# Kernel tuning notes

Measured on AMD Instinct MI355X. Metric: run time of the kernel, lower is better.

The kernel has to match this reference:

```python
import jax, jax.numpy as jnp
import numpy as np

B, T, E, H, D = 256, 77, 1280, 20, 64
SCALE = D ** -0.5
NEG = -1e9


def setup_inputs() -> dict:
    key = jax.random.key(0)
    ks = jax.random.split(key, 32)
    w = lambda k, shape, s=0.02: jax.random.normal(k, shape, dtype=jnp.float32) * s
    causal = jnp.triu(jnp.full((T, T), NEG, dtype=jnp.float32), k=1)
    causal_mask = jnp.broadcast_to(causal[None, None], (B, 1, T, T))
    return {
        'hidden_states': jax.random.normal(ks[0], (B, T, E), dtype=jnp.float32),
        'embeds': jax.random.normal(ks[1], (B, T, E), dtype=jnp.float32),
        'causal_mask': causal_mask,
        'q_w': w(ks[2], (E, E)), 'q_b': w(ks[3], (E,)),
        'k_w': w(ks[4], (E, E)), 'k_b': w(ks[5], (E,)),
        'v_w': w(ks[6], (E, E)), 'v_b': w(ks[7], (E,)),
        'o_w': w(ks[8], (E, E)), 'o_b': w(ks[9], (E,)),
        'ka_w': w(ks[10], (E, E)) * 0.01, 'ka_b': w(ks[11], (E,)) * 0.001,
        'va_w': w(ks[12], (E, E)) * 0.01, 'va_b': w(ks[13], (E,)) * 0.001,
        'zc1_w': w(ks[14], (E, E)), 'zc1_b': w(ks[15], (E,)),
        'zt1_w': w(ks[16], (T, 2 * T)), 'zt1_b': w(ks[17], (T,)),
        'zc2_w': w(ks[18], (E, E)), 'zc2_b': w(ks[19], (E,)),
        'zt2_w': w(ks[20], (T, T)), 'zt2_b': w(ks[21], (T,)),
    }


def _heads(x):
    # (B, S, E) -> (B, H, S, D)
    return x.reshape(B, -1, H, D).transpose(0, 2, 1, 3)


def _attend(q, k, v, mask=None):
    # q,k,v: (B,H,*,D); returns (B,T,E)
    logits = jnp.einsum('bhtd,bhsd->bhts', q, k)
    if mask is not None:
        logits = logits + mask  # mask: (B,1,T,S)
    probs = jax.nn.softmax(logits, axis=-1)  # dropout p=0 in eval
    ctx = jnp.einsum('bhts,bhsd->bhtd', probs, v)
    return ctx.transpose(0, 2, 1, 3).reshape(B, T, E)


def _zipper(x, zc1_w, zc1_b, zt1_w, zt1_b, zc2_w, zc2_b, zt2_w, zt2_b):
    # token/channel mixer: (B, 2T, E) -> (B, T, E)
    x = jax.nn.gelu(x @ zc1_w.T + zc1_b)              # channel: E -> hidden E
    x = jnp.swapaxes(x, 1, 2)                          # (B, E, 2T)
    x = jax.nn.gelu(x @ zt1_w.T + zt1_b)               # tokens: 2T -> T
    x = jnp.swapaxes(x, 1, 2)                          # (B, T, E)
    x = x @ zc2_w.T + zc2_b                            # channel: E -> E
    x = jnp.swapaxes(x, 1, 2) @ zt2_w.T + zt2_b        # tokens: T -> T
    return jnp.swapaxes(x, 1, 2)


def reference(hidden_states, embeds, causal_mask,
              q_w, q_b, k_w, k_b, v_w, v_b, o_w, o_b,
              ka_w, ka_b, va_w, va_b,
              zc1_w, zc1_b, zt1_w, zt1_b, zc2_w, zc2_b, zt2_w, zt2_b):
    q = _heads((hidden_states @ q_w.T + q_b) * SCALE)
    k = _heads(hidden_states @ k_w.T + k_b)
    v = _heads(hidden_states @ v_w.T + v_b)
    attn_output = _attend(q, k, v, causal_mask)  # self-attention pass

    # adapter cross-attention pass (shared query)
    ka = _heads(embeds @ ka_w.T + ka_b)
    va = _heads(embeds @ va_w.T + va_b)
    attn_output_adapter = _attend(q, ka, va, None)

    zipped = _zipper(jnp.concatenate([attn_output_adapter, attn_output], axis=1),
                     zc1_w, zc1_b, zt1_w, zt1_b, zc2_w, zc2_b, zt2_w, zt2_b)
    attn_output = attn_output + zipped
    return attn_output @ o_w.T + o_b
```

## Files before the change

kernel.cpp:

```cpp
#include <hip/hip_runtime.h>
#include <stdint.h>

#define B_    256
#define T_    77
#define E_    1280
#define H_    20
#define T2_   154
#define MTOK  19712
#define MTOK2 39424

typedef float f32x4 __attribute__((ext_vector_type(4)));
typedef short bf16x8 __attribute__((ext_vector_type(8)));

__device__ inline float bf2f(short s) {
    return __uint_as_float(((unsigned)(unsigned short)s) << 16);
}
__device__ inline short f2bf(float f) {
    unsigned u = __float_as_uint(f);
    u += 0x7fff + ((u >> 16) & 1);
    return (short)(u >> 16);
}
__device__ inline float gelu_tanh(float x) {
    float x3 = x * x * x;
    return 0.5f * x * (1.0f + tanhf(0.7978845608028654f * (x + 0.044715f * x3)));
}

__global__ void cast_f32_bf16(const float* __restrict__ in, short* __restrict__ out, int n4) {
    int i = blockIdx.x * blockDim.x + threadIdx.x;
    int stride = gridDim.x * blockDim.x;
    for (; i < n4; i += stride) {
        float4 v = reinterpret_cast<const float4*>(in)[i];
        short4 o;
        o.x = f2bf(v.x); o.y = f2bf(v.y); o.z = f2bf(v.z); o.w = f2bf(v.w);
        reinterpret_cast<short4*>(out)[i] = o;
    }
}

__global__ void cast8_f32_bf16(const float* __restrict__ s0, const float* __restrict__ s1,
                               const float* __restrict__ s2, const float* __restrict__ s3,
                               const float* __restrict__ s4, const float* __restrict__ s5,
                               const float* __restrict__ s6, const float* __restrict__ s7,
                               short* __restrict__ out) {
    const int per = E_ * E_ / 4;
    int i = blockIdx.x * blockDim.x + threadIdx.x;
    int stride = gridDim.x * blockDim.x;
    for (; i < 8 * per; i += stride) {
        int w = i / per, j = i - w * per;
        const float* src = w == 0 ? s0 : w == 1 ? s1 : w == 2 ? s2 : w == 3 ? s3
                         : w == 4 ? s4 : w == 5 ? s5 : w == 6 ? s6 : s7;
        float4 v = reinterpret_cast<const float4*>(src)[j];
        short4 o;
        o.x = f2bf(v.x); o.y = f2bf(v.y); o.z = f2bf(v.z); o.w = f2bf(v.w);
        reinterpret_cast<short4*>(out)[i] = o;
    }
}

__global__ void pad_weight(const float* __restrict__ W, short* __restrict__ Wp,
                           int rows, int cols, int KP) {
    int i = blockIdx.x * 256 + threadIdx.x;
    if (i >= 80 * KP) return;
    int t = i / KP, s = i - t * KP;
    Wp[i] = (t < rows && s < cols) ? f2bf(W[t * cols + s]) : (short)0;
}

template<int NSEG, int EPI>
__global__ __launch_bounds__(512, 2)
void qgemm(const short* __restrict__ A, const short* __restrict__ W,
           const float* __restrict__ b0, const float* __restrict__ b1,
           const float* __restrict__ b2,
           short* __restrict__ o0, short* __restrict__ o1, short* __restrict__ o2,
           float s0) {
    const int K = E_;
    const int NT = K / 64;
    __shared__ short As[2 * 2 * 8192];
    __shared__ short Bs[2 * 2 * 8192];
    const int tid = threadIdx.x;
    const int wave = tid >> 6, lane = tid & 63;
    const int wr = wave >> 2, wc = wave & 3;

    const int nwg = gridDim.x;
    const int qq = nwg >> 3, rr = nwg & 7;
    const int x = blockIdx.x & 7, ii = blockIdx.x >> 3;
    const int L = (x < rr ? x * (qq + 1) : rr * (qq + 1) + (x - rr) * qq) + ii;
    const int PB = nwg / NSEG;
    const int seg = L / PB;
    const int rem = L - seg * PB;
    const int bm = rem / 5, bnl = rem % 5;

    const long arow0 = (long)bm * 256;
    const long brow0 = (long)seg * E_ + bnl * 256;

    const int rsub = lane >> 3;
    const int colswz = (((lane & 7) ^ rsub) & 7) * 8;
    const int swz = (lane & 7) << 3;

    f32x4 acc[8][4] = {};

    auto STAGE_A = [&](int par, int half, int kt) {
#pragma unroll
        for (int i = 0; i < 2; ++i) {
            int chunk = i * 8 + wave;
            int row = chunk * 8 + rsub;
            const short* ga = A + (arow0 + half * 128 + row) * K + kt * 64 + colswz;
            __builtin_amdgcn_global_load_lds(
                (const __attribute__((address_space(1))) unsigned int*)ga,
                (__attribute__((address_space(3))) unsigned int*)
                    &As[par * 16384 + half * 8192 + chunk * 512], 16, 0, 0);
        }
    };
    auto STAGE_B = [&](int par, int half, int kt) {
#pragma unroll
        for (int i = 0; i < 2; ++i) {
            int chunk = i * 8 + wave;
            int row = chunk * 8 + rsub;
            const short* gb = W + (brow0 + half * 128 + row) * K + kt * 64 + colswz;
            __builtin_amdgcn_global_load_lds(
                (const __attribute__((address_space(1))) unsigned int*)gb,
                (__attribute__((address_space(3))) unsigned int*)
                    &Bs[par * 16384 + half * 8192 + chunk * 512], 16, 0, 0);
        }
    };

    bf16x8 Afr[4][2], Bfr[2][2];
    auto LDA = [&](int par, int hm) {
#pragma unroll
        for (int mi = 0; mi < 4; ++mi)
#pragma unroll
            for (int kk = 0; kk < 2; ++kk)
                Afr[mi][kk] = *reinterpret_cast<const bf16x8*>(
                    &As[par * 16384 + hm * 8192 +
                        (((wr * 64 + mi * 16 + (lane & 15)) * 64 + kk * 32 +
                          (lane >> 4) * 8) ^ swz)]);
    };
    auto LDB = [&](int par, int hn) {
#pragma unroll
        for (int nj = 0; nj < 2; ++nj)
#pragma unroll
            for (int kk = 0; kk < 2; ++kk)
                Bfr[nj][kk] = *reinterpret_cast<const bf16x8*>(
                    &Bs[par * 16384 + hn * 8192 +
                        (((wc * 32 + nj * 16 + (lane & 15)) * 64 + kk * 32 +
                          (lane >> 4) * 8) ^ swz)]);
    };
    auto MFMA16 = [&](int hm, int hn) {
        __builtin_amdgcn_s_setprio(1);
#pragma unroll
        for (int mi = 0; mi < 4; ++mi)
#pragma unroll
            for (int nj = 0; nj < 2; ++nj)
#pragma unroll
                for (int kk = 0; kk < 2; ++kk)
                    acc[hm * 4 + mi][hn * 2 + nj] =
                        __builtin_amdgcn_mfma_f32_16x16x32_bf16(
                            Afr[mi][kk], Bfr[nj][kk], acc[hm * 4 + mi][hn * 2 + nj],
                            0, 0, 0);
        __builtin_amdgcn_s_setprio(0);
    };

    STAGE_A(0, 0, 0); STAGE_B(0, 0, 0); STAGE_B(0, 1, 0); STAGE_A(0, 1, 0);

    for (int t = 0; t < NT - 1; ++t) {
        const int par = t & 1, nxt = par ^ 1;
        asm volatile("s_waitcnt vmcnt(4)" ::: "memory");
        __builtin_amdgcn_s_barrier(); __builtin_amdgcn_sched_barrier(0);
        LDA(par, 0); LDB(par, 0);
        STAGE_A(nxt, 0, t + 1);
        MFMA16(0, 0);
        asm volatile("s_waitcnt vmcnt(4)" ::: "memory");
        __builtin_amdgcn_s_barrier(); __builtin_amdgcn_sched_barrier(0);
        LDB(par, 1);
        STAGE_B(nxt, 0, t + 1);
        MFMA16(0, 1);
        asm volatile("s_waitcnt vmcnt(4)" ::: "memory");
        __builtin_amdgcn_s_barrier(); __builtin_amdgcn_sched_barrier(0);
        LDA(par, 1); LDB(par, 0);
        STAGE_B(nxt, 1, t + 1);
        MFMA16(1, 0);
        __builtin_amdgcn_s_barrier(); __builtin_amdgcn_sched_barrier(0);
        LDB(par, 1);
        STAGE_A(nxt, 1, t + 1);
        MFMA16(1, 1);
    }
    {
        const int par = (NT - 1) & 1;
        asm volatile("s_waitcnt vmcnt(4)" ::: "memory");
        __builtin_amdgcn_s_barrier(); __builtin_amdgcn_sched_barrier(0);
        LDA(par, 0); LDB(par, 0);
        MFMA16(0, 0);
        asm volatile("s_waitcnt vmcnt(2)" ::: "memory");
        __builtin_amdgcn_s_barrier(); __builtin_amdgcn_sched_barrier(0);
        LDB(par, 1);
        MFMA16(0, 1);
        asm volatile("s_waitcnt vmcnt(0)" ::: "memory");
        __builtin_amdgcn_s_barrier(); __builtin_amdgcn_sched_barrier(0);
        LDA(par, 1); LDB(par, 0);
        MFMA16(1, 0);
        __builtin_amdgcn_s_barrier(); __builtin_amdgcn_sched_barrier(0);
        LDB(par, 1);
        MFMA16(1, 1);
    }

    const float* bias = seg == 0 ? b0 : (seg == 1 ? b1 : b2);
    short* out = seg == 0 ? o0 : (seg == 1 ? o1 : o2);
    const float scl = (EPI == 0 && seg == 0) ? s0 : 1.f;
#pragma unroll
    for (int hm = 0; hm < 2; ++hm)
#pragma unroll
        for (int mi = 0; mi < 4; ++mi)
#pragma unroll
            for (int hn = 0; hn < 2; ++hn)
#pragma unroll
                for (int nj = 0; nj < 2; ++nj) {
                    int ncol = bnl * 256 + hn * 128 + wc * 32 + nj * 16 + (lane & 15);
                    float bv = bias[ncol];
#pragma unroll
                    for (int r = 0; r < 4; ++r) {
                        long grow = arow0 + hm * 128 + wr * 64 + mi * 16 +
                                    (lane >> 4) * 4 + r;
                        float v = acc[hm * 4 + mi][hn * 2 + nj][r] + bv;
                        if (EPI == 2) v = gelu_tanh(v);
                        else v *= scl;
                        out[grow * E_ + ncol] = f2bf(v);
                    }
                }
}

#define GEMM_CORE(A_, W_, KDIM, ACC)                                                   \
    const int rsub = lane >> 3;                                                        \
    const int col  = (((lane & 7) ^ rsub) & 7) * 8;                                    \
    const int swz  = (lane & 7) << 3;                                                  \
    for (int kt = 0; kt < (KDIM); kt += 64) {                                          \
        __syncthreads();                                                               \
        _Pragma("unroll")                                                              \
        for (int i = 0; i < 4; ++i) {                                                  \
            int chunk = i * 4 + wave;                                                  \
            int row = chunk * 8 + rsub;                                                \
            const short* ga = (A_) + (arow0 + row) * (KDIM) + kt + col;                \
            const short* gb = (W_) + (brow0 + row) * (KDIM) + kt + col;                \
            __builtin_amdgcn_global_load_lds(                                          \
                (const __attribute__((address_space(1))) unsigned int*)ga,             \
                (__attribute__((address_space(3))) unsigned int*)&Als[chunk * 512],    \
                16, 0, 0);                                                             \
            __builtin_amdgcn_global_load_lds(                                          \
                (const __attribute__((address_space(1))) unsigned int*)gb,             \
                (__attribute__((address_space(3))) unsigned int*)&Bls[chunk * 512],    \
                16, 0, 0);                                                             \
        }                                                                              \
        __syncthreads();                                                               \
        _Pragma("unroll")                                                              \
        for (int kk = 0; kk < 2; ++kk) {                                               \
            bf16x8 af[4], bfr[4];                                                      \
            _Pragma("unroll")                                                          \
            for (int mi = 0; mi < 4; ++mi)                                             \
                af[mi] = *reinterpret_cast<const bf16x8*>(                             \
                    &Als[(((wm + mi * 16 + (lane & 15)) * 64 + kk * 32 +               \
                           (lane >> 4) * 8)) ^ swz]);                                  \
            _Pragma("unroll")                                                          \
            for (int nj = 0; nj < 4; ++nj)                                             \
                bfr[nj] = *reinterpret_cast<const bf16x8*>(                            \
                    &Bls[(((wn + nj * 16 + (lane & 15)) * 64 + kk * 32 +               \
                           (lane >> 4) * 8)) ^ swz]);                                  \
            _Pragma("unroll")                                                          \
            for (int mi = 0; mi < 4; ++mi)                                             \
                _Pragma("unroll")                                                      \
                for (int nj = 0; nj < 4; ++nj)                                         \
                    ACC[mi][nj] = __builtin_amdgcn_mfma_f32_16x16x32_bf16(             \
                        af[mi], bfr[nj], ACC[mi][nj], 0, 0, 0);                        \
        }                                                                              \
    }

template<int EPI>
__global__ void gemm_bt(const short* __restrict__ A, const short* __restrict__ W,
                        const float* __restrict__ bias, void* __restrict__ Cout,
                        int K) {
    const int N = E_;
    const int NBN = E_ / 128;
    __shared__ short Als[128 * 64];
    __shared__ short Bls[128 * 64];
    const int tid  = threadIdx.x;
    const int wave = tid >> 6, lane = tid & 63;

    const int nwg = gridDim.x;
    const int qq = nwg >> 3, rr = nwg & 7;
    const int x = blockIdx.x & 7, ii = blockIdx.x >> 3;
    const int L = (x < rr ? x * (qq + 1) : rr * (qq + 1) + (x - rr) * qq) + ii;
    const int bm = L / NBN, bn = L % NBN;

    const int wm = (wave >> 1) * 64, wn = (wave & 1) * 64;
    f32x4 acc[4][4] = {};
    const long arow0 = (long)bm * 128;
    const long brow0 = (long)bn * 128;

    GEMM_CORE(A, W, K, acc)

#pragma unroll
    for (int mi = 0; mi < 4; ++mi) {
#pragma unroll
        for (int nj = 0; nj < 4; ++nj) {
            int gcol = bn * 128 + wn + nj * 16 + (lane & 15);
            float bv = bias[gcol];
#pragma unroll
            for (int r = 0; r < 4; ++r) {
                long grow = arow0 + wm + mi * 16 + (lane >> 4) * 4 + r;
                float v = acc[mi][nj][r] + bv;
                if (EPI == 3) ((float*)Cout)[grow * N + gcol] = v;
                else          ((short*)Cout)[grow * N + gcol] = f2bf(v);
            }
        }
    }
}

template<int SIN, int KP, int PS, bool GELU, bool RESID>
__global__ void mixer_mfma(const short* __restrict__ IN, const short* __restrict__ Wp,
                           const float* __restrict__ bias, const short* __restrict__ Cat,
                           short* __restrict__ OUT) {
    __shared__ short lsT[64 * PS];
    const int e0 = blockIdx.x * 64;
    const int b  = blockIdx.y;
    const int tid = threadIdx.x, wave = tid >> 6, lane = tid & 63;

    const int eg = tid & 7;
    const int sl = tid >> 3;
    for (int sb = sl; sb < KP; sb += 32) {
        if (sb < SIN) {
            bf16x8 v = *reinterpret_cast<const bf16x8*>(
                &IN[((long)b * SIN + sb) * E_ + e0 + eg * 8]);
#pragma unroll
            for (int i = 0; i < 8; ++i)
                lsT[(eg * 8 + i) * PS + sb] = v[i];
        } else {
#pragma unroll
            for (int i = 0; i < 8; ++i)
                lsT[(eg * 8 + i) * PS + sb] = 0;
        }
    }
    __syncthreads();

    const int ebase = wave * 16;
    f32x4 acc[5] = {};
#pragma unroll
    for (int ks = 0; ks < KP / 32; ++ks) {
        bf16x8 bfr = *reinterpret_cast<const bf16x8*>(
            &lsT[(ebase + (lane & 15)) * PS + ks * 32 + (lane >> 4) * 8]);
#pragma unroll
        for (int mt = 0; mt < 5; ++mt) {
            bf16x8 af = *reinterpret_cast<const bf16x8*>(
                &Wp[(mt * 16 + (lane & 15)) * KP + ks * 32 + (lane >> 4) * 8]);
            acc[mt] = __builtin_amdgcn_mfma_f32_16x16x32_bf16(af, bfr, acc[mt], 0, 0, 0);
        }
    }

    const int e = e0 + ebase + (lane & 15);
#pragma unroll
    for (int mt = 0; mt < 5; ++mt) {
#pragma unroll
        for (int r = 0; r < 4; ++r) {
            int t = mt * 16 + (lane >> 4) * 4 + r;
            if (t < T_) {
                float v = acc[mt][r] + bias[t];
                if (GELU) v = gelu_tanh(v);
                if (RESID) v += bf2f(Cat[((long)b * T2_ + T_ + t) * E_ + e]);
                OUT[((long)b * T_ + t) * E_ + e] = f2bf(v);
            }
        }
    }
}

#define ASTR 104
__global__ __launch_bounds__(64, 1)
void attn_mfma(const short* __restrict__ Qm,
               const short* __restrict__ Km, const short* __restrict__ Vm,
               const short* __restrict__ KAm, const short* __restrict__ VAm,
               short* __restrict__ Cat) {
    __shared__ short pls[80 * ASTR];
    __shared__ short vt[64 * ASTR];
    const int hh = blockIdx.x;
    const int b = hh / H_, h = hh % H_;
    const int lane = threadIdx.x & 63;
    const int colbase = lane & 15, g = lane >> 4;
    const long base = ((long)b * T_) * E_ + h * 64;

    for (int pass = 0; pass < 2; ++pass) {
        const short* Kp = pass ? KAm : Km;
        const short* Vp = pass ? VAm : Vm;
        const bool causal = (pass == 0);
        const int rowoff = pass ? 0 : T_;

        {
            int4 z = {0, 0, 0, 0};
#pragma unroll
            for (int it = 0; it < 4; ++it) {
                int idx = it * 64 + lane;
                int row = idx >> 2, cb = idx & 3;
                *reinterpret_cast<int4*>(&vt[row * ASTR + 64 + cb * 8]) = z;
            }
#pragma unroll
            for (int it = 0; it < 3; ++it) {
                int idx = it * 64 + lane;
                if (idx < 160) {
                    int row = idx >> 1, cb = idx & 1;
                    *reinterpret_cast<int4*>(&pls[row * ASTR + 80 + cb * 8]) = z;
                }
            }
        }

        {
            const short* vb = Vp + base + (long)lane * E_;
#pragma unroll
            for (int dg = 0; dg < 8; ++dg) {
                bf16x8 v = *reinterpret_cast<const bf16x8*>(vb + dg * 8);
#pragma unroll
                for (int i = 0; i < 8; ++i) vt[(dg * 8 + i) * ASTR + lane] = v[i];
            }
            if (lane < T_ - 64) {
                const short* vb2 = Vp + base + (long)(64 + lane) * E_;
#pragma unroll
                for (int dg = 0; dg < 8; ++dg) {
                    bf16x8 v = *reinterpret_cast<const bf16x8*>(vb2 + dg * 8);
#pragma unroll
                    for (int i = 0; i < 8; ++i) vt[(dg * 8 + i) * ASTR + 64 + lane] = v[i];
                }
            }
        }

        f32x4 sacc[5][5] = {};
#pragma unroll
        for (int kk = 0; kk < 2; ++kk) {
            bf16x8 qf[5];
#pragma unroll
            for (int mi = 0; mi < 5; ++mi) {
                int t = mi * 16 + colbase; t = t > 76 ? 76 : t;
                qf[mi] = *reinterpret_cast<const bf16x8*>(
                    Qm + base + (long)t * E_ + kk * 32 + g * 8);
            }
#pragma unroll
            for (int nj = 0; nj < 5; ++nj) {
                int s = nj * 16 + colbase; s = s > 76 ? 76 : s;
                bf16x8 kf = *reinterpret_cast<const bf16x8*>(
                    Kp + base + (long)s * E_ + kk * 32 + g * 8);
#pragma unroll
                for (int mi = 0; mi < 5; ++mi)
                    sacc[mi][nj] = __builtin_amdgcn_mfma_f32_16x16x32_bf16(
                        qf[mi], kf, sacc[mi][nj], 0, 0, 0);
            }
        }

        float inv[5][4];
#pragma unroll
        for (int mi = 0; mi < 5; ++mi) {
#pragma unroll
            for (int r = 0; r < 4; ++r) {
                int t = mi * 16 + g * 4 + r;
                float mx = -3.0e38f;
#pragma unroll
                for (int nj = 0; nj < 5; ++nj) {
                    int s = nj * 16 + colbase;
                    bool ok = causal ? (s <= t) : (s < T_);
                    if (ok) mx = fmaxf(mx, sacc[mi][nj][r]);
                }
#pragma unroll
                for (int o = 1; o <= 8; o <<= 1) mx = fmaxf(mx, __shfl_xor(mx, o));
                float sum = 0.f;
#pragma unroll
                for (int nj = 0; nj < 5; ++nj) {
                    int s = nj * 16 + colbase;
                    bool ok = causal ? (s <= t) : (s < T_);
                    float pv = ok ? __expf(sacc[mi][nj][r] - mx) : 0.f;
                    sacc[mi][nj][r] = pv;
                    sum += pv;
                }
#pragma unroll
                for (int o = 1; o <= 8; o <<= 1) sum += __shfl_xor(sum, o);
                inv[mi][r] = 1.0f / sum;
            }
        }

#pragma unroll
        for (int mi = 0; mi < 5; ++mi)
#pragma unroll
            for (int nj = 0; nj < 5; ++nj)
#pragma unroll
                for (int r = 0; r < 4; ++r)
                    pls[(mi * 16 + g * 4 + r) * ASTR + nj * 16 + colbase] =
                        f2bf(sacc[mi][nj][r]);

        f32x4 cacc[5][4] = {};
#pragma unroll
        for (int ks = 0; ks < 3; ++ks) {
            bf16x8 pa[5];
#pragma unroll
            for (int mi = 0; mi < 5; ++mi)
                pa[mi] = *reinterpret_cast<const bf16x8*>(
                    &pls[(mi * 16 + colbase) * ASTR + ks * 32 + g * 8]);
#pragma unroll
            for (int nd = 0; nd < 4; ++nd) {
                bf16x8 vf = *reinterpret_cast<const bf16x8*>(
                    &vt[(nd * 16 + colbase) * ASTR + ks * 32 + g * 8]);
#pragma unroll
                for (int mi = 0; mi < 5; ++mi)
                    cacc[mi][nd] = __builtin_amdgcn_mfma_f32_16x16x32_bf16(
                        pa[mi], vf, cacc[mi][nd], 0, 0, 0);
            }
        }

#pragma unroll
        for (int mi = 0; mi < 5; ++mi)
#pragma unroll
            for (int nd = 0; nd < 4; ++nd)
#pragma unroll
                for (int r = 0; r < 4; ++r) {
                    int t = mi * 16 + g * 4 + r;
                    if (t < T_) {
                        float val = cacc[mi][nd][r] * inv[mi][r];
                        Cat[((long)b * T2_ + rowoff + t) * E_ + h * 64 + nd * 16 + colbase] =
                            f2bf(val);
                    }
                }
    }
}

extern "C" void kernel_launch(void* const* d_in, const int* in_sizes, int n_in,
                              void* d_out, int out_size, void* d_ws, size_t ws_size,
                              hipStream_t stream) {
    const float* hidden = (const float*)d_in[0];
    const float* embeds = (const float*)d_in[1];
    const float* q_w  = (const float*)d_in[3];  const float* q_b  = (const float*)d_in[4];
    const float* k_w  = (const float*)d_in[5];  const float* k_b  = (const float*)d_in[6];
    const float* v_w  = (const float*)d_in[7];  const float* v_b  = (const float*)d_in[8];
    const float* o_w  = (const float*)d_in[9];  const float* o_b  = (const float*)d_in[10];
    const float* ka_w = (const float*)d_in[11]; const float* ka_b = (const float*)d_in[12];
    const float* va_w = (const float*)d_in[13]; const float* va_b = (const float*)d_in[14];
    const float* zc1_w = (const float*)d_in[15]; const float* zc1_b = (const float*)d_in[16];
    const float* zt1_w = (const float*)d_in[17]; const float* zt1_b = (const float*)d_in[18];
    const float* zc2_w = (const float*)d_in[19]; const float* zc2_b = (const float*)d_in[20];
    const float* zt2_w = (const float*)d_in[21]; const float* zt2_b = (const float*)d_in[22];

    char* ws = (char*)d_ws;
    const size_t WSZ = (size_t)E_ * E_ * 2;
    const size_t ASZ = (size_t)MTOK * E_ * 2;
    short* Wq  = (short*)(ws + 0 * WSZ);
    short* Wka = (short*)(ws + 3 * WSZ);
    short* Wz1 = (short*)(ws + 5 * WSZ);
    short* Wz2 = (short*)(ws + 6 * WSZ);
    short* Wo  = (short*)(ws + 7 * WSZ);
    char* p = ws + 8 * WSZ;
    short* Ahs  = (short*)p; p += ASZ;
    short* Aemb = (short*)p; p += ASZ;
    short* Qb   = (short*)p; p += ASZ;
    short* Kb   = (short*)p; p += ASZ;
    short* Vb   = (short*)p; p += ASZ;
    short* KAb  = (short*)p; p += ASZ;
    short* VAb  = (short*)p; p += ASZ;
    short* Wz1p = (short*)p; p += 80 * 160 * 2;
    short* Wz2p = (short*)p; p += 80 * 96 * 2;
    short* CAT = Ahs;
    short* Y   = KAb;
    short* X2  = Qb;
    short* X3  = Kb;
    short* S   = Vb;

    if (ws_size < (size_t)(p - ws)) return;

    cast_f32_bf16<<<2048, 256, 0, stream>>>(hidden, Ahs,  MTOK * E_ / 4);
    cast_f32_bf16<<<2048, 256, 0, stream>>>(embeds, Aemb, MTOK * E_ / 4);
    cast8_f32_bf16<<<2048, 256, 0, stream>>>(q_w, k_w, v_w, ka_w, va_w, zc1_w, zc2_w, o_w,
                                             Wq);
    pad_weight<<<(80 * 160 + 255) / 256, 256, 0, stream>>>(zt1_w, Wz1p, 77, 154, 160);
    pad_weight<<<(80 * 96 + 255) / 256, 256, 0, stream>>>(zt2_w, Wz2p, 77, 77, 96);

    const int gQKV  = (MTOK / 256) * (3 * E_ / 256);
    const int gKAVA = (MTOK / 256) * (2 * E_ / 256);
    const int gZC1  = (MTOK2 / 256) * (E_ / 256);
    const int g154  = (MTOK / 128) * (E_ / 128);
    qgemm<3, 0><<<gQKV, 512, 0, stream>>>(Ahs, Wq, q_b, k_b, v_b,
                                          Qb, Kb, Vb, 0.125f);
    qgemm<2, 0><<<gKAVA, 512, 0, stream>>>(Aemb, Wka, ka_b, va_b, va_b,
                                           KAb, VAb, VAb, 1.f);
    attn_mfma<<<B_ * H_, 64, 0, stream>>>(Qb, Kb, Vb, KAb, VAb, CAT);
    qgemm<1, 2><<<gZC1, 512, 0, stream>>>(CAT, Wz1, zc1_b, zc1_b, zc1_b,
                                          Y, Y, Y, 1.f);
    mixer_mfma<154, 160, 168, true, false><<<dim3(E_ / 64, B_), 256, 0, stream>>>(
        Y, Wz1p, zt1_b, nullptr, X2);
    gemm_bt<0><<<g154, 256, 0, stream>>>(X2, Wz2, zc2_b, X3, E_);
    mixer_mfma<77, 96, 104, false, true><<<dim3(E_ / 64, B_), 256, 0, stream>>>(
        X3, Wz2p, zt2_b, CAT, S);
    gemm_bt<3><<<g154, 256, 0, stream>>>(S, Wo, o_b, (float*)d_out, E_);
}
```

Baseline: 1.154 ms.

## Double-buffer A/B register fragments and reorder quadrant MFMAs to cut LDS reloads

```diff
diff --git a/kernel.cpp b/kernel.cpp
--- a/kernel.cpp
+++ b/kernel.cpp
@@ -95,6 +95,7 @@
     const int swz = (lane & 7) << 3;
 
     f32x4 acc[8][4] = {};
+    bf16x8 AfA[4][2], AfB[4][2], Bf0[2][2], Bf1[2][2];
 
     auto STAGE_A = [&](int par, int half, int kt) {
 #pragma unroll
@@ -120,29 +121,27 @@
                     &Bs[par * 16384 + half * 8192 + chunk * 512], 16, 0, 0);
         }
     };
-
-    bf16x8 Afr[4][2], Bfr[2][2];
-    auto LDA = [&](int par, int hm) {
+    auto LDA = [&](bf16x8 (&dst)[4][2], int par, int hm) {
 #pragma unroll
         for (int mi = 0; mi < 4; ++mi)
 #pragma unroll
             for (int kk = 0; kk < 2; ++kk)
-                Afr[mi][kk] = *reinterpret_cast<const bf16x8*>(
+                dst[mi][kk] = *reinterpret_cast<const bf16x8*>(
                     &As[par * 16384 + hm * 8192 +
                         (((wr * 64 + mi * 16 + (lane & 15)) * 64 + kk * 32 +
                           (lane >> 4) * 8) ^ swz)]);
     };
-    auto LDB = [&](int par, int hn) {
+    auto LDB = [&](bf16x8 (&dst)[2][2], int par, int hn) {
 #pragma unroll
         for (int nj = 0; nj < 2; ++nj)
 #pragma unroll
             for (int kk = 0; kk < 2; ++kk)
-                Bfr[nj][kk] = *reinterpret_cast<const bf16x8*>(
+                dst[nj][kk] = *reinterpret_cast<const bf16x8*>(
                     &Bs[par * 16384 + hn * 8192 +
                         (((wc * 32 + nj * 16 + (lane & 15)) * 64 + kk * 32 +
                           (lane >> 4) * 8) ^ swz)]);
     };
-    auto MFMA16 = [&](int hm, int hn) {
+    auto MFMA16 = [&](int hm, bf16x8 (&Af)[4][2], bf16x8 (&Bf)[2][2], int hn) {
         __builtin_amdgcn_s_setprio(1);
 #pragma unroll
         for (int mi = 0; mi < 4; ++mi)
@@ -152,52 +151,55 @@
                 for (int kk = 0; kk < 2; ++kk)
                     acc[hm * 4 + mi][hn * 2 + nj] =
                         __builtin_amdgcn_mfma_f32_16x16x32_bf16(
-                            Afr[mi][kk], Bfr[nj][kk], acc[hm * 4 + mi][hn * 2 + nj],
+                            Af[mi][kk], Bf[nj][kk], acc[hm * 4 + mi][hn * 2 + nj],
                             0, 0, 0);
         __builtin_amdgcn_s_setprio(0);
     };
 
     STAGE_A(0, 0, 0); STAGE_B(0, 0, 0); STAGE_B(0, 1, 0); STAGE_A(0, 1, 0);
+    asm volatile("s_waitcnt vmcnt(6)" ::: "memory");
+    __builtin_amdgcn_s_barrier(); __builtin_amdgcn_sched_barrier(0);
+    LDA(AfA, 0, 0);
 
     for (int t = 0; t < NT - 1; ++t) {
         const int par = t & 1, nxt = par ^ 1;
         asm volatile("s_waitcnt vmcnt(4)" ::: "memory");
         __builtin_amdgcn_s_barrier(); __builtin_amdgcn_sched_barrier(0);
-        LDA(par, 0); LDB(par, 0);
+        LDB(Bf0, par, 0);
         STAGE_A(nxt, 0, t + 1);
-        MFMA16(0, 0);
+        MFMA16(0, AfA, Bf0, 0);
         asm volatile("s_waitcnt vmcnt(4)" ::: "memory");
         __builtin_amdgcn_s_barrier(); __builtin_amdgcn_sched_barrier(0);
-        LDB(par, 1);
+        LDB(Bf1, par, 1);
         STAGE_B(nxt, 0, t + 1);
-        MFMA16(0, 1);
+        MFMA16(0, AfA, Bf1, 1);
         asm volatile("s_waitcnt vmcnt(4)" ::: "memory");
         __builtin_amdgcn_s_barrier(); __builtin_amdgcn_sched_barrier(0);
-        LDA(par, 1); LDB(par, 0);
+        LDA(AfB, par, 1);
         STAGE_B(nxt, 1, t + 1);
-        MFMA16(1, 0);
-        __builtin_amdgcn_s_barrier(); __builtin_amdgcn_sched_barrier(0);
-        LDB(par, 1);
+        MFMA16(1, AfB, Bf1, 1);
+        asm volatile("s_waitcnt vmcnt(4)" ::: "memory");
+        __builtin_amdgcn_s_barrier(); __builtin_amdgcn_sched_barrier(0);
+        LDA(AfA, nxt, 0);
         STAGE_A(nxt, 1, t + 1);
-        MFMA16(1, 1);
+        MFMA16(1, AfB, Bf0, 0);
     }
     {
         const int par = (NT - 1) & 1;
         asm volatile("s_waitcnt vmcnt(4)" ::: "memory");
         __builtin_amdgcn_s_barrier(); __builtin_amdgcn_sched_barrier(0);
-        LDA(par, 0); LDB(par, 0);
-        MFMA16(0, 0);
+        LDB(Bf0, par, 0);
+        MFMA16(0, AfA, Bf0, 0);
         asm volatile("s_waitcnt vmcnt(2)" ::: "memory");
         __builtin_amdgcn_s_barrier(); __builtin_amdgcn_sched_barrier(0);
-        LDB(par, 1);
-        MFMA16(0, 1);
+        LDB(Bf1, par, 1);
+        MFMA16(0, AfA, Bf1, 1);
         asm volatile("s_waitcnt vmcnt(0)" ::: "memory");
         __builtin_amdgcn_s_barrier(); __builtin_amdgcn_sched_barrier(0);
-        LDA(par, 1); LDB(par, 0);
-        MFMA16(1, 0);
-        __builtin_amdgcn_s_barrier(); __builtin_amdgcn_sched_barrier(0);
-        LDB(par, 1);
-        MFMA16(1, 1);
+        LDA(AfB, par, 1);
+        MFMA16(1, AfB, Bf1, 1);
+        __builtin_amdgcn_s_barrier(); __builtin_amdgcn_sched_barrier(0);
+        MFMA16(1, AfB, Bf0, 0);
     }
 
     const float* bias = seg == 0 ? b0 : (seg == 1 ? b1 : b2);
```

Result: slower. 1.218 ms (+5.6%).
